# Performance work log

Hardware: AMD Instinct MI355X
Metric: run time of the kernel (lower is better)

Reference implementation:

```python
import jax, jax.numpy as jnp
from jax import lax
import numpy as np

DN = ('NCHW', 'OIHW', 'NCHW')
PAD = [(1, 1), (1, 1)]  # padding=1 each side
STRIDE = (1, 1)


def setup_inputs() -> dict:
    key = jax.random.key(0)
    k0, k1, k2, k3, k4, k5 = jax.random.split(key, 6)
    B, Cin, Cout, H, W, K, FES = 32, 96, 144, 56, 56, 3, 3
    fan_main = Cin * K * K
    fan_extra = FES * K * K
    x = jax.random.normal(k0, (B, Cin, H, W), dtype=jnp.float32)
    extra_inputs = jax.random.normal(k1, (B, Cout * FES), dtype=jnp.float32)
    Wm = jax.random.normal(k2, (Cout, Cin, K, K), dtype=jnp.float32) / np.sqrt(fan_main)
    bm = jax.random.normal(k3, (Cout,), dtype=jnp.float32) * 0.01
    Wx = jax.random.normal(k4, (Cout, FES, K, K), dtype=jnp.float32) / np.sqrt(fan_extra)
    bx = jax.random.normal(k5, (Cout,), dtype=jnp.float32) * 0.01
    return {"x": x, "extra_inputs": extra_inputs, "Wm": Wm, "bm": bm, "Wx": Wx, "bx": bx}


def reference(x, extra_inputs, Wm, bm, Wx, bx):
    # main path: standard conv + bias
    main = lax.conv_general_dilated(x, Wm, STRIDE, PAD, dimension_numbers=DN)
    main = main + bm[None, :, None, None]

    B = x.shape[0]
    Cout, FES, kh, kw = Wx.shape
    H2, W2 = main.shape[2], main.shape[3]

    # Extra path: each extra conv operates on a spatially-constant map, so
    # conv(const_c) = const_c * conv(ones). Compute per-(out,fes)-kernel response
    # to a ones map once (captures zero-padding boundary effects exactly),
    # then combine via a batched einsum — collapsing the per-channel loop.
    ones = jnp.ones((1, 1, x.shape[2], x.shape[3]), dtype=x.dtype)
    M = lax.conv_general_dilated(
        ones, Wx.reshape(Cout * FES, 1, kh, kw), STRIDE, PAD, dimension_numbers=DN
    )  # [1, Cout*FES, H2, W2]
    M = M.reshape(Cout, FES, H2, W2)

    extra = extra_inputs.reshape(B, Cout, FES)
    extra_out = jnp.einsum('bif,ifhw->bihw', extra, M) + bx[None, :, None, None]

    return main + extra_out
```

## Files before the change

kernel.cpp:

```cpp
#include <hip/hip_runtime.h>
#include <hip/hip_bf16.h>

#define B_    32
#define CIN   96
#define COUT  144
#define H_    56
#define W_    56
#define HW    3136
#define NPIX  100352
#define KTOT  864
#define MT    256
#define TAPSZ (COUT*CIN)
#define W2    58
#define PLANE (W2*W2)
#define XTP_SHORTS ((size_t)B_ * PLANE * CIN)

typedef short  short8  __attribute__((ext_vector_type(8)));
typedef float  floatx4 __attribute__((ext_vector_type(4)));

__device__ __forceinline__ unsigned short f2bf(float f) {
    union { float f; unsigned int u; } v; v.f = f;
    unsigned int u = v.u;
    return (unsigned short)((u + 0x7FFFu + ((u >> 16) & 1u)) >> 16);
}

__device__ __forceinline__ void glds16(const void* g, void* l) {
    __builtin_amdgcn_global_load_lds(
        (const __attribute__((address_space(1))) unsigned int*)g,
        (__attribute__((address_space(3))) unsigned int*)l, 16, 0, 0);
}

#define TB 1568
#define WB 486
#define EB 18
#define ZB 342
__global__ __launch_bounds__(256) void prep_all(const float* __restrict__ x,
                                                unsigned short* __restrict__ xTp,
                                                const float* __restrict__ Wm,
                                                unsigned short* __restrict__ Wt,
                                                const float* __restrict__ extra,
                                                const float* __restrict__ Wx,
                                                const float* __restrict__ bm,
                                                const float* __restrict__ bx,
                                                float* __restrict__ E) {
    __shared__ __align__(16) unsigned short tile[64][CIN + 8];
    int blk = blockIdx.x;
    int t = threadIdx.x;
    if (blk < TB) {
        int b   = blk / 49;
        int hw0 = (blk % 49) * 64;
        const float* xb = x + (size_t)b * CIN * HW;
        for (int i = t; i < CIN * 16; i += 256) {
            int ci = i >> 4, seg = i & 15;
            float4 v = *(const float4*)(xb + (size_t)ci * HW + hw0 + seg * 4);
            int hwl = seg * 4;
            tile[hwl + 0][ci] = f2bf(v.x);
            tile[hwl + 1][ci] = f2bf(v.y);
            tile[hwl + 2][ci] = f2bf(v.z);
            tile[hwl + 3][ci] = f2bf(v.w);
        }
        __syncthreads();
        int row = t >> 2, part = t & 3;
        int hw = hw0 + row;
        int h  = hw / W_;
        int w  = hw - h * W_;
        const uint4* s = (const uint4*)&tile[row][part * 24];
        uint4* d = (uint4*)(xTp + ((size_t)((b * W2 + h + 1) * W2 + (w + 1))) * CIN
                                + part * 24);
        d[0] = s[0]; d[1] = s[1]; d[2] = s[2];
    } else if (blk < TB + WB) {
        int i = (blk - TB) * 256 + t;
        int tap = i / 13824;
        int r1  = i - tap * 13824;
        int g   = r1 / 1152;
        int r2  = r1 - g * 1152;
        int co  = r2 >> 3;
        int e   = r2 & 7;
        int ci  = g * 8 + e;
        Wt[i] = f2bf(Wm[((size_t)co * CIN + ci) * 9 + tap]);
    } else if (blk < TB + WB + EB) {
        int i = (blk - TB - WB) * 256 + t;
        int b = i / COUT, co = i - b * COUT;
        float base = bm[co] + bx[co];
        float m[3][3] = {{0,0,0},{0,0,0},{0,0,0}};
        for (int f = 0; f < 3; ++f) {
            float e = extra[(size_t)b * (COUT * 3) + co * 3 + f];
            const float* w = Wx + ((size_t)co * 3 + f) * 9;
            for (int rc = 0; rc < 3; ++rc) {
                int kh0 = (rc == 0) ? 1 : 0;
                int kh1 = (rc == 2) ? 1 : 2;
                for (int cc = 0; cc < 3; ++cc) {
                    int kw0 = (cc == 0) ? 1 : 0;
                    int kw1 = (cc == 2) ? 1 : 2;
                    float s = 0.f;
                    for (int kh = kh0; kh <= kh1; ++kh)
                        for (int kw = kw0; kw <= kw1; ++kw)
                            s += w[kh * 3 + kw];
                    m[rc][cc] += e * s;
                }
            }
        }
        float* dst = E + (size_t)i * 9;
        for (int rc = 0; rc < 3; ++rc)
            for (int cc = 0; cc < 3; ++cc)
                dst[rc * 3 + cc] = base + m[rc][cc];
    } else {
        int i = (blk - TB - WB - EB) * 256 + t;
        int b = i / 2736;
        int r = i - b * 2736;
        size_t base_b = (size_t)b * PLANE * CIN;
        size_t addr;
        if (r < 696) {
            addr = base_b + (size_t)r * 8;
        } else if (r < 1392) {
            addr = base_b + (size_t)57 * W2 * CIN + (size_t)(r - 696) * 8;
        } else if (r < 2064) {
            int r2 = r - 1392;
            int h = 1 + r2 / 12, u = r2 - (r2 / 12) * 12;
            addr = base_b + (size_t)(h * W2) * CIN + (size_t)u * 8;
        } else {
            int r2 = r - 2064;
            int h = 1 + r2 / 12, u = r2 - (r2 / 12) * 12;
            addr = base_b + (size_t)(h * W2 + 57) * CIN + (size_t)u * 8;
        }
        *(short8*)(xTp + addr) = (short8){0, 0, 0, 0, 0, 0, 0, 0};
    }
}

__global__ __launch_bounds__(256, 2) void conv_gemm(const unsigned short* __restrict__ xTp,
                                                    const unsigned short* __restrict__ Wt,
                                                    const float* __restrict__ E,
                                                    float* __restrict__ out) {
    __shared__ __align__(16) unsigned short Bs[2 * TAPSZ];

    int tid = threadIdx.x;
    int wv = tid >> 6, lane = tid & 63;
    int r16 = lane & 15, q = lane >> 4;
    int pixBase = blockIdx.x * MT;

    floatx4 acc[4][9];
    #pragma unroll
    for (int m = 0; m < 4; ++m)
        #pragma unroll
        for (int n = 0; n < 9; ++n)
            acc[m][n] = (floatx4){0.f, 0.f, 0.f, 0.f};

    int aOff[4];
    #pragma unroll
    for (int ms = 0; ms < 4; ++ms) {
        int p = pixBase + wv * 64 + ms * 16 + r16;
        int b = p / HW;
        int hw = p - b * HW;
        int h = hw / W_;
        int w = hw - h * W_;
        aOff[ms] = ((b * W2 + h + 1) * W2 + (w + 1)) * CIN + q * 8;
    }

    const bool bTail = (tid < 192);

    const unsigned short* BpBase = Bs + (q * COUT + r16) * 8;

    short8 a[4][3];

    {
        const unsigned short* wsrc = Wt;
        #pragma unroll
        for (int j = 0; j < 6; ++j)
            glds16(wsrc + tid * 8 + j * 2048, (void*)(Bs + tid * 8 + j * 2048));
        if (bTail)
            glds16(wsrc + tid * 8 + 6 * 2048, (void*)(Bs + tid * 8 + 6 * 2048));
        const unsigned short* bT = xTp + (ptrdiff_t)((-1 * W2 - 1) * CIN);
        #pragma unroll
        for (int ms = 0; ms < 4; ++ms)
            #pragma unroll
            for (int ks = 0; ks < 3; ++ks)
                a[ms][ks] = *(const short8*)(bT + aOff[ms] + ks * 32);
    }
    __syncthreads();

    #pragma unroll 1
    for (int tap = 0; tap < 9; ++tap) {
        const int cur = tap & 1, nxt = cur ^ 1;
        const bool pf = (tap < 8);

        const int tap2 = tap + (pf ? 1 : 0);
        const int r3   = tap2 / 3;
        const int dh2  = r3 - 1, dw2 = tap2 - r3 * 3 - 1;
        const unsigned short* bT = xTp + (ptrdiff_t)((dh2 * W2 + dw2) * CIN);
        if (pf) {
            const unsigned short* wsrc = Wt + tap2 * TAPSZ;
            unsigned short* bd = Bs + nxt * TAPSZ;
            #pragma unroll
            for (int j = 0; j < 6; ++j)
                glds16(wsrc + tid * 8 + j * 2048, (void*)(bd + tid * 8 + j * 2048));
            if (bTail)
                glds16(wsrc + tid * 8 + 6 * 2048, (void*)(bd + tid * 8 + 6 * 2048));
        }

        const unsigned short* Bp = BpBase + cur * TAPSZ;
        #pragma unroll
        for (int ks = 0; ks < 3; ++ks) {
            #pragma unroll
            for (int n3 = 0; n3 < 3; ++n3) {
                short8 b0 = *(const short8*)(Bp + ks * 4608 + (n3 * 3 + 0) * 128);
                short8 b1 = *(const short8*)(Bp + ks * 4608 + (n3 * 3 + 1) * 128);
                short8 b2 = *(const short8*)(Bp + ks * 4608 + (n3 * 3 + 2) * 128);
                #pragma unroll
                for (int ms = 0; ms < 4; ++ms)
                    acc[ms][n3 * 3 + 0] = __builtin_amdgcn_mfma_f32_16x16x32_bf16(
                        a[ms][ks], b0, acc[ms][n3 * 3 + 0], 0, 0, 0);
                #pragma unroll
                for (int ms = 0; ms < 4; ++ms)
                    acc[ms][n3 * 3 + 1] = __builtin_amdgcn_mfma_f32_16x16x32_bf16(
                        a[ms][ks], b1, acc[ms][n3 * 3 + 1], 0, 0, 0);
                #pragma unroll
                for (int ms = 0; ms < 4; ++ms)
                    acc[ms][n3 * 3 + 2] = __builtin_amdgcn_mfma_f32_16x16x32_bf16(
                        a[ms][ks], b2, acc[ms][n3 * 3 + 2], 0, 0, 0);
            }
            #pragma unroll
            for (int ms = 0; ms < 4; ++ms)
                a[ms][ks] = *(const short8*)(bT + aOff[ms] + ks * 32);
        }

        __syncthreads();
    }

    #pragma unroll
    for (int ms = 0; ms < 4; ++ms) {
        int p0 = pixBase + wv * 64 + ms * 16 + q * 4;
        int b  = p0 / HW;
        int hw0 = p0 - b * HW;
        int h = hw0 / W_;
        int w0 = hw0 - h * W_;
        int rc = (h == 0) ? 0 : ((h == H_ - 1) ? 2 : 1);
        int cc0 = (w0 == 0) ? 0 : ((w0 == W_ - 1) ? 2 : 1);
        int cc1 = (w0 + 1 == W_ - 1) ? 2 : 1;
        int cc2 = (w0 + 2 == W_ - 1) ? 2 : 1;
        int cc3 = (w0 + 3 == W_ - 1) ? 2 : 1;
        const float* Ebase = E + (size_t)b * COUT * 9 + rc * 3;
        float* outB = out + (size_t)b * COUT * HW + hw0;
        #pragma unroll
        for (int n = 0; n < 9; ++n) {
            int co = n * 16 + r16;
            const float* Eb = Ebase + co * 9;
            float4 v;
            v.x = acc[ms][n][0] + Eb[cc0];
            v.y = acc[ms][n][1] + Eb[cc1];
            v.z = acc[ms][n][2] + Eb[cc2];
            v.w = acc[ms][n][3] + Eb[cc3];
            *(float4*)(outB + (size_t)co * HW) = v;
        }
    }
}

extern "C" void kernel_launch(void* const* d_in, const int* in_sizes, int n_in,
                              void* d_out, int out_size, void* d_ws, size_t ws_size,
                              hipStream_t stream) {
    const float* x     = (const float*)d_in[0];
    const float* extra = (const float*)d_in[1];
    const float* Wm    = (const float*)d_in[2];
    const float* bm    = (const float*)d_in[3];
    const float* Wx    = (const float*)d_in[4];
    const float* bx    = (const float*)d_in[5];
    float* out = (float*)d_out;

    const size_t XT_BYTES = XTP_SHORTS * 2;
    const size_t WT_BYTES = (size_t)COUT * KTOT * 2;
    const size_t E_BYTES  = (size_t)B_ * COUT * 9 * 4;
    if (ws_size < XT_BYTES + WT_BYTES + E_BYTES) return;

    unsigned short* xTp = (unsigned short*)d_ws;
    unsigned short* Wt  = (unsigned short*)((char*)d_ws + XT_BYTES);
    float*          E   = (float*)((char*)d_ws + XT_BYTES + WT_BYTES);

    prep_all<<<TB + WB + EB + ZB, 256, 0, stream>>>(x, xTp, Wm, Wt, extra, Wx, bm, bx, E);
    conv_gemm<<<NPIX / MT, 256, 0, stream>>>(xTp, Wt, E, out);
}
```

Before: 150.3 us.

## Use 512-thread blocks with smaller per-wave tiles and double-buffered A registers

Doubles the block size to 8 waves, each now computing 32 pixels instead of 64, so each CU holds more waves for latency hiding while the block tile stays the same. The per-tap A fragments are now held in two register sets (aA/aB) that alternate, so the next tap's global loads are issued before the current tap's MFMAs. The tap loop is unrolled in pairs through a macro, and the final tap skips its barrier. In exchange, each wave reads the full B tile from LDS for half as many MFMAs, which doubles LDS read traffic per unit of compute.

Result: no change. 152.7 us (+1.6%).

```diff
diff --git a/kernel.cpp b/kernel.cpp
--- a/kernel.cpp
+++ b/kernel.cpp
@@ -127,7 +127,53 @@
     }
 }
 
-__global__ __launch_bounds__(256, 2) void conv_gemm(const unsigned short* __restrict__ xTp,
+#define TAP_BODY(TAP, CUR, ACUR, ANXT, PF)                                        \
+    do {                                                                          \
+        if (PF) {                                                                 \
+            const int tap2 = (TAP) + 1;                                           \
+            const int r3   = tap2 / 3;                                            \
+            const int dh2  = r3 - 1, dw2 = tap2 - r3 * 3 - 1;                     \
+            const unsigned short* wsrc = Wt + tap2 * TAPSZ;                       \
+            unsigned short* bd = Bs + (1 - (CUR)) * TAPSZ;                        \
+            _Pragma("unroll")                                                     \
+            for (int j = 0; j < 3; ++j)                                           \
+                glds16(wsrc + (tid + j * 512) * 8,                                \
+                       (void*)(bd + (tid + j * 512) * 8));                        \
+            if (bTail)                                                            \
+                glds16(wsrc + (1536 + tid) * 8, (void*)(bd + (1536 + tid) * 8));  \
+            const unsigned short* bT = xTp + (ptrdiff_t)((dh2 * W2 + dw2) * CIN); \
+            _Pragma("unroll")                                                     \
+            for (int ms = 0; ms < 2; ++ms)                                        \
+                _Pragma("unroll")                                                 \
+                for (int ks = 0; ks < 3; ++ks)                                    \
+                    ANXT[ms][ks] = *(const short8*)(bT + aOff[ms] + ks * 32);     \
+        }                                                                         \
+        const unsigned short* Bp = BpBase + (CUR) * TAPSZ;                        \
+        _Pragma("unroll")                                                         \
+        for (int ks = 0; ks < 3; ++ks) {                                          \
+            _Pragma("unroll")                                                     \
+            for (int n3 = 0; n3 < 3; ++n3) {                                      \
+                short8 b0 = *(const short8*)(Bp + ks * 4608 + (n3 * 3 + 0) * 128);\
+                short8 b1 = *(const short8*)(Bp + ks * 4608 + (n3 * 3 + 1) * 128);\
+                short8 b2 = *(const short8*)(Bp + ks * 4608 + (n3 * 3 + 2) * 128);\
+                _Pragma("unroll")                                                 \
+                for (int ms = 0; ms < 2; ++ms)                                    \
+                    acc[ms][n3 * 3 + 0] = __builtin_amdgcn_mfma_f32_16x16x32_bf16(\
+                        ACUR[ms][ks], b0, acc[ms][n3 * 3 + 0], 0, 0, 0);          \
+                _Pragma("unroll")                                                 \
+                for (int ms = 0; ms < 2; ++ms)                                    \
+                    acc[ms][n3 * 3 + 1] = __builtin_amdgcn_mfma_f32_16x16x32_bf16(\
+                        ACUR[ms][ks], b1, acc[ms][n3 * 3 + 1], 0, 0, 0);          \
+                _Pragma("unroll")                                                 \
+                for (int ms = 0; ms < 2; ++ms)                                    \
+                    acc[ms][n3 * 3 + 2] = __builtin_amdgcn_mfma_f32_16x16x32_bf16(\
+                        ACUR[ms][ks], b2, acc[ms][n3 * 3 + 2], 0, 0, 0);          \
+            }                                                                     \
+        }                                                                         \
+        if (PF) __syncthreads();                                                  \
+    } while (0)
+
+__global__ __launch_bounds__(512, 2) void conv_gemm(const unsigned short* __restrict__ xTp,
                                                     const unsigned short* __restrict__ Wt,
                                                     const float* __restrict__ E,
                                                     float* __restrict__ out) {
@@ -138,17 +184,17 @@
     int r16 = lane & 15, q = lane >> 4;
     int pixBase = blockIdx.x * MT;
 
-    floatx4 acc[4][9];
+    floatx4 acc[2][9];
     #pragma unroll
-    for (int m = 0; m < 4; ++m)
+    for (int m = 0; m < 2; ++m)
         #pragma unroll
         for (int n = 0; n < 9; ++n)
             acc[m][n] = (floatx4){0.f, 0.f, 0.f, 0.f};
 
-    int aOff[4];
+    int aOff[2];
     #pragma unroll
-    for (int ms = 0; ms < 4; ++ms) {
-        int p = pixBase + wv * 64 + ms * 16 + r16;
+    for (int ms = 0; ms < 2; ++ms) {
+        int p = pixBase + wv * 32 + ms * 16 + r16;
         int b = p / HW;
         int hw = p - b * HW;
         int h = hw / W_;
@@ -160,75 +206,35 @@
 
     const unsigned short* BpBase = Bs + (q * COUT + r16) * 8;
 
-    short8 a[4][3];
+    short8 aA[2][3], aB[2][3];
 
     {
         const unsigned short* wsrc = Wt;
         #pragma unroll
-        for (int j = 0; j < 6; ++j)
-            glds16(wsrc + tid * 8 + j * 2048, (void*)(Bs + tid * 8 + j * 2048));
+        for (int j = 0; j < 3; ++j)
+            glds16(wsrc + (tid + j * 512) * 8, (void*)(Bs + (tid + j * 512) * 8));
         if (bTail)
-            glds16(wsrc + tid * 8 + 6 * 2048, (void*)(Bs + tid * 8 + 6 * 2048));
+            glds16(wsrc + (1536 + tid) * 8, (void*)(Bs + (1536 + tid) * 8));
         const unsigned short* bT = xTp + (ptrdiff_t)((-1 * W2 - 1) * CIN);
         #pragma unroll
-        for (int ms = 0; ms < 4; ++ms)
+        for (int ms = 0; ms < 2; ++ms)
             #pragma unroll
             for (int ks = 0; ks < 3; ++ks)
-                a[ms][ks] = *(const short8*)(bT + aOff[ms] + ks * 32);
+                aA[ms][ks] = *(const short8*)(bT + aOff[ms] + ks * 32);
     }
     __syncthreads();
 
     #pragma unroll 1
-    for (int tap = 0; tap < 9; ++tap) {
-        const int cur = tap & 1, nxt = cur ^ 1;
-        const bool pf = (tap < 8);
-
-        const int tap2 = tap + (pf ? 1 : 0);
-        const int r3   = tap2 / 3;
-        const int dh2  = r3 - 1, dw2 = tap2 - r3 * 3 - 1;
-        const unsigned short* bT = xTp + (ptrdiff_t)((dh2 * W2 + dw2) * CIN);
-        if (pf) {
-            const unsigned short* wsrc = Wt + tap2 * TAPSZ;
-            unsigned short* bd = Bs + nxt * TAPSZ;
-            #pragma unroll
-            for (int j = 0; j < 6; ++j)
-                glds16(wsrc + tid * 8 + j * 2048, (void*)(bd + tid * 8 + j * 2048));
-            if (bTail)
-                glds16(wsrc + tid * 8 + 6 * 2048, (void*)(bd + tid * 8 + 6 * 2048));
-        }
-
-        const unsigned short* Bp = BpBase + cur * TAPSZ;
-        #pragma unroll
-        for (int ks = 0; ks < 3; ++ks) {
-            #pragma unroll
-            for (int n3 = 0; n3 < 3; ++n3) {
-                short8 b0 = *(const short8*)(Bp + ks * 4608 + (n3 * 3 + 0) * 128);
-                short8 b1 = *(const short8*)(Bp + ks * 4608 + (n3 * 3 + 1) * 128);
-                short8 b2 = *(const short8*)(Bp + ks * 4608 + (n3 * 3 + 2) * 128);
-                #pragma unroll
-                for (int ms = 0; ms < 4; ++ms)
-                    acc[ms][n3 * 3 + 0] = __builtin_amdgcn_mfma_f32_16x16x32_bf16(
-                        a[ms][ks], b0, acc[ms][n3 * 3 + 0], 0, 0, 0);
-                #pragma unroll
-                for (int ms = 0; ms < 4; ++ms)
-                    acc[ms][n3 * 3 + 1] = __builtin_amdgcn_mfma_f32_16x16x32_bf16(
-                        a[ms][ks], b1, acc[ms][n3 * 3 + 1], 0, 0, 0);
-                #pragma unroll
-                for (int ms = 0; ms < 4; ++ms)
-                    acc[ms][n3 * 3 + 2] = __builtin_amdgcn_mfma_f32_16x16x32_bf16(
-                        a[ms][ks], b2, acc[ms][n3 * 3 + 2], 0, 0, 0);
-            }
-            #pragma unroll
-            for (int ms = 0; ms < 4; ++ms)
-                a[ms][ks] = *(const short8*)(bT + aOff[ms] + ks * 32);
-        }
-
-        __syncthreads();
-    }
+    for (int t2 = 0; t2 < 4; ++t2) {
+        const int tapE = 2 * t2;
+        TAP_BODY(tapE,     0, aA, aB, true);
+        TAP_BODY(tapE + 1, 1, aB, aA, true);
+    }
+    TAP_BODY(8, 0, aA, aB, false);
 
     #pragma unroll
-    for (int ms = 0; ms < 4; ++ms) {
-        int p0 = pixBase + wv * 64 + ms * 16 + q * 4;
+    for (int ms = 0; ms < 2; ++ms) {
+        int p0 = pixBase + wv * 32 + ms * 16 + q * 4;
         int b  = p0 / HW;
         int hw0 = p0 - b * HW;
         int h = hw0 / W_;
@@ -275,5 +281,5 @@
     float*          E   = (float*)((char*)d_ws + XT_BYTES + WT_BYTES);
 
     prep_all<<<TB + WB + EB + ZB, 256, 0, stream>>>(x, xTp, Wm, Wt, extra, Wx, bm, bx, E);
-    conv_gemm<<<NPIX / MT, 256, 0, stream>>>(xTp, Wt, E, out);
-}
+    conv_gemm<<<NPIX / MT, 512, 0, stream>>>(xTp, Wt, E, out);
+}
```

## Stage five weight taps in LDS per 512-thread block to cut barriers

Applied to the files above, without the earlier changes.

The block grows to 512 threads and 512 pixels per tile. Instead of double-buffering one weight tap per iteration, the kernel loads weight taps 0-4 into LDS up front, computes them, then reloads the remaining four taps in a single phase. This drops per-tap barriers and async loads from the inner loop. In exchange it uses about 138KB of LDS, which limits occupancy to one block per CU. The grid also shrinks to 196 blocks, and the mid-kernel weight reload is fully exposed with no overlap.

Result: no change. 152.1 us (+1.2%).

```diff
diff --git a/kernel.cpp b/kernel.cpp
--- a/kernel.cpp
+++ b/kernel.cpp
@@ -9,7 +9,7 @@
 #define HW    3136
 #define NPIX  100352
 #define KTOT  864
-#define MT    256
+#define MT    512
 #define TAPSZ (COUT*CIN)
 #define W2    58
 #define PLANE (W2*W2)
@@ -127,11 +127,40 @@
     }
 }
 
-__global__ __launch_bounds__(256, 2) void conv_gemm(const unsigned short* __restrict__ xTp,
+#define MFMA16(A, B, C) __builtin_amdgcn_mfma_f32_16x16x32_bf16(A, B, C, 0, 0, 0)
+
+#define TAP_COMPUTE(BP, BT, PF)                                                   \
+    do {                                                                          \
+        _Pragma("unroll")                                                         \
+        for (int ks = 0; ks < 3; ++ks) {                                          \
+            _Pragma("unroll")                                                     \
+            for (int n3 = 0; n3 < 3; ++n3) {                                      \
+                short8 b0 = *(const short8*)((BP) + ks * 4608 + (n3 * 3 + 0) * 128);\
+                short8 b1 = *(const short8*)((BP) + ks * 4608 + (n3 * 3 + 1) * 128);\
+                short8 b2 = *(const short8*)((BP) + ks * 4608 + (n3 * 3 + 2) * 128);\
+                _Pragma("unroll")                                                 \
+                for (int ms = 0; ms < 4; ++ms)                                    \
+                    acc[ms][n3 * 3 + 0] = MFMA16(a[ms][ks], b0, acc[ms][n3 * 3 + 0]);\
+                _Pragma("unroll")                                                 \
+                for (int ms = 0; ms < 4; ++ms)                                    \
+                    acc[ms][n3 * 3 + 1] = MFMA16(a[ms][ks], b1, acc[ms][n3 * 3 + 1]);\
+                _Pragma("unroll")                                                 \
+                for (int ms = 0; ms < 4; ++ms)                                    \
+                    acc[ms][n3 * 3 + 2] = MFMA16(a[ms][ks], b2, acc[ms][n3 * 3 + 2]);\
+            }                                                                     \
+            if (PF) {                                                             \
+                _Pragma("unroll")                                                 \
+                for (int ms = 0; ms < 4; ++ms)                                    \
+                    a[ms][ks] = *(const short8*)((BT) + aOff[ms] + ks * 32);      \
+            }                                                                     \
+        }                                                                         \
+    } while (0)
+
+__global__ __launch_bounds__(512, 2) void conv_gemm(const unsigned short* __restrict__ xTp,
                                                     const unsigned short* __restrict__ Wt,
                                                     const float* __restrict__ E,
                                                     float* __restrict__ out) {
-    __shared__ __align__(16) unsigned short Bs[2 * TAPSZ];
+    __shared__ __align__(16) unsigned short Bs[5 * TAPSZ];
 
     int tid = threadIdx.x;
     int wv = tid >> 6, lane = tid & 63;
@@ -156,19 +185,16 @@
         aOff[ms] = ((b * W2 + h + 1) * W2 + (w + 1)) * CIN + q * 8;
     }
 
-    const bool bTail = (tid < 192);
-
     const unsigned short* BpBase = Bs + (q * COUT + r16) * 8;
 
     short8 a[4][3];
 
     {
-        const unsigned short* wsrc = Wt;
-        #pragma unroll
-        for (int j = 0; j < 6; ++j)
-            glds16(wsrc + tid * 8 + j * 2048, (void*)(Bs + tid * 8 + j * 2048));
-        if (bTail)
-            glds16(wsrc + tid * 8 + 6 * 2048, (void*)(Bs + tid * 8 + 6 * 2048));
+        #pragma unroll
+        for (int j = 0; j < 16; ++j)
+            glds16(Wt + (tid + j * 512) * 8, (void*)(Bs + (tid + j * 512) * 8));
+        if (tid < 448)
+            glds16(Wt + (tid + 16 * 512) * 8, (void*)(Bs + (tid + 16 * 512) * 8));
         const unsigned short* bT = xTp + (ptrdiff_t)((-1 * W2 - 1) * CIN);
         #pragma unroll
         for (int ms = 0; ms < 4; ++ms)
@@ -179,51 +205,36 @@
     __syncthreads();
 
     #pragma unroll 1
-    for (int tap = 0; tap < 9; ++tap) {
-        const int cur = tap & 1, nxt = cur ^ 1;
-        const bool pf = (tap < 8);
-
-        const int tap2 = tap + (pf ? 1 : 0);
-        const int r3   = tap2 / 3;
-        const int dh2  = r3 - 1, dw2 = tap2 - r3 * 3 - 1;
-        const unsigned short* bT = xTp + (ptrdiff_t)((dh2 * W2 + dw2) * CIN);
-        if (pf) {
-            const unsigned short* wsrc = Wt + tap2 * TAPSZ;
-            unsigned short* bd = Bs + nxt * TAPSZ;
-            #pragma unroll
-            for (int j = 0; j < 6; ++j)
-                glds16(wsrc + tid * 8 + j * 2048, (void*)(bd + tid * 8 + j * 2048));
-            if (bTail)
-                glds16(wsrc + tid * 8 + 6 * 2048, (void*)(bd + tid * 8 + 6 * 2048));
-        }
-
-        const unsigned short* Bp = BpBase + cur * TAPSZ;
-        #pragma unroll
-        for (int ks = 0; ks < 3; ++ks) {
-            #pragma unroll
-            for (int n3 = 0; n3 < 3; ++n3) {
-                short8 b0 = *(const short8*)(Bp + ks * 4608 + (n3 * 3 + 0) * 128);
-                short8 b1 = *(const short8*)(Bp + ks * 4608 + (n3 * 3 + 1) * 128);
-                short8 b2 = *(const short8*)(Bp + ks * 4608 + (n3 * 3 + 2) * 128);
-                #pragma unroll
-                for (int ms = 0; ms < 4; ++ms)
-                    acc[ms][n3 * 3 + 0] = __builtin_amdgcn_mfma_f32_16x16x32_bf16(
-                        a[ms][ks], b0, acc[ms][n3 * 3 + 0], 0, 0, 0);
-                #pragma unroll
-                for (int ms = 0; ms < 4; ++ms)
-                    acc[ms][n3 * 3 + 1] = __builtin_amdgcn_mfma_f32_16x16x32_bf16(
-                        a[ms][ks], b1, acc[ms][n3 * 3 + 1], 0, 0, 0);
-                #pragma unroll
-                for (int ms = 0; ms < 4; ++ms)
-                    acc[ms][n3 * 3 + 2] = __builtin_amdgcn_mfma_f32_16x16x32_bf16(
-                        a[ms][ks], b2, acc[ms][n3 * 3 + 2], 0, 0, 0);
-            }
-            #pragma unroll
-            for (int ms = 0; ms < 4; ++ms)
-                a[ms][ks] = *(const short8*)(bT + aOff[ms] + ks * 32);
-        }
-
-        __syncthreads();
+    for (int tap = 0; tap < 5; ++tap) {
+        int t1 = tap + 1;
+        int r3 = (t1 * 11) >> 5;
+        const unsigned short* bT = xTp + (ptrdiff_t)(((r3 - 1) * W2 + (t1 - r3 * 3 - 1)) * CIN);
+        const unsigned short* Bp = BpBase + tap * TAPSZ;
+        TAP_COMPUTE(Bp, bT, true);
+    }
+
+    __syncthreads();
+    {
+        const unsigned short* wsrc = Wt + 5 * TAPSZ;
+        #pragma unroll
+        for (int j = 0; j < 13; ++j)
+            glds16(wsrc + (tid + j * 512) * 8, (void*)(Bs + (tid + j * 512) * 8));
+        if (tid < 256)
+            glds16(wsrc + (tid + 13 * 512) * 8, (void*)(Bs + (tid + 13 * 512) * 8));
+    }
+    __syncthreads();
+
+    #pragma unroll 1
+    for (int tap = 5; tap < 8; ++tap) {
+        int t1 = tap + 1;
+        int r3 = (t1 * 11) >> 5;
+        const unsigned short* bT = xTp + (ptrdiff_t)(((r3 - 1) * W2 + (t1 - r3 * 3 - 1)) * CIN);
+        const unsigned short* Bp = BpBase + (tap - 5) * TAPSZ;
+        TAP_COMPUTE(Bp, bT, true);
+    }
+    {
+        const unsigned short* Bp = BpBase + 3 * TAPSZ;
+        TAP_COMPUTE(Bp, xTp, false);
     }
 
     #pragma unroll
@@ -275,5 +286,5 @@
     float*          E   = (float*)((char*)d_ws + XT_BYTES + WT_BYTES);
 
     prep_all<<<TB + WB + EB + ZB, 256, 0, stream>>>(x, xTp, Wm, Wt, extra, Wx, bm, bx, E);
-    conv_gemm<<<NPIX / MT, 256, 0, stream>>>(xTp, Wt, E, out);
-}
+    conv_gemm<<<NPIX / MT, 512, 0, stream>>>(xTp, Wt, E, out);
+}
```

## Halve pixel tile and single-buffer weight tile in LDS to raise occupancy

Applied to the files above, without the earlier changes.

Cuts the per-block pixel tile from 256 to 128, halving the accumulator and A-fragment registers per wave. The weight double buffer in LDS becomes a single buffer that is loaded and synchronised at the top of every tap, and the launch bound goes from 2 to 3 blocks per CU. The goal is more resident waves to hide latency, at the cost of losing the overlap between the next tap's weight prefetch and the MFMAs. It also doubles how many times each block reloads the full weight set, relative to the number of pixels processed.

Measured after the change: 150.1 us. No clear change (-0.1%).

```diff
diff --git a/kernel.cpp b/kernel.cpp
--- a/kernel.cpp
+++ b/kernel.cpp
@@ -9,7 +9,7 @@
 #define HW    3136
 #define NPIX  100352
 #define KTOT  864
-#define MT    256
+#define MT    128
 #define TAPSZ (COUT*CIN)
 #define W2    58
 #define PLANE (W2*W2)
@@ -127,28 +127,30 @@
     }
 }
 
-__global__ __launch_bounds__(256, 2) void conv_gemm(const unsigned short* __restrict__ xTp,
+#define MFMA16(A, B, C) __builtin_amdgcn_mfma_f32_16x16x32_bf16(A, B, C, 0, 0, 0)
+
+__global__ __launch_bounds__(256, 3) void conv_gemm(const unsigned short* __restrict__ xTp,
                                                     const unsigned short* __restrict__ Wt,
                                                     const float* __restrict__ E,
                                                     float* __restrict__ out) {
-    __shared__ __align__(16) unsigned short Bs[2 * TAPSZ];
+    __shared__ __align__(16) unsigned short Bs[TAPSZ];
 
     int tid = threadIdx.x;
     int wv = tid >> 6, lane = tid & 63;
     int r16 = lane & 15, q = lane >> 4;
     int pixBase = blockIdx.x * MT;
 
-    floatx4 acc[4][9];
+    floatx4 acc[2][9];
     #pragma unroll
-    for (int m = 0; m < 4; ++m)
+    for (int m = 0; m < 2; ++m)
         #pragma unroll
         for (int n = 0; n < 9; ++n)
             acc[m][n] = (floatx4){0.f, 0.f, 0.f, 0.f};
 
-    int aOff[4];
+    int aOff[2];
     #pragma unroll
-    for (int ms = 0; ms < 4; ++ms) {
-        int p = pixBase + wv * 64 + ms * 16 + r16;
+    for (int ms = 0; ms < 2; ++ms) {
+        int p = pixBase + wv * 32 + ms * 16 + r16;
         int b = p / HW;
         int hw = p - b * HW;
         int h = hw / W_;
@@ -160,66 +162,51 @@
 
     const unsigned short* BpBase = Bs + (q * COUT + r16) * 8;
 
-    short8 a[4][3];
+    short8 a[2][3];
 
     {
-        const unsigned short* wsrc = Wt;
-        #pragma unroll
-        for (int j = 0; j < 6; ++j)
-            glds16(wsrc + tid * 8 + j * 2048, (void*)(Bs + tid * 8 + j * 2048));
-        if (bTail)
-            glds16(wsrc + tid * 8 + 6 * 2048, (void*)(Bs + tid * 8 + 6 * 2048));
-        const unsigned short* bT = xTp + (ptrdiff_t)((-1 * W2 - 1) * CIN);
-        #pragma unroll
-        for (int ms = 0; ms < 4; ++ms)
+        const unsigned short* bT = xTp - (ptrdiff_t)((W2 + 1) * CIN);
+        #pragma unroll
+        for (int ms = 0; ms < 2; ++ms)
             #pragma unroll
             for (int ks = 0; ks < 3; ++ks)
                 a[ms][ks] = *(const short8*)(bT + aOff[ms] + ks * 32);
     }
-    __syncthreads();
 
     #pragma unroll 1
     for (int tap = 0; tap < 9; ++tap) {
-        const int cur = tap & 1, nxt = cur ^ 1;
-        const bool pf = (tap < 8);
-
-        const int tap2 = tap + (pf ? 1 : 0);
-        const int r3   = tap2 / 3;
-        const int dh2  = r3 - 1, dw2 = tap2 - r3 * 3 - 1;
-        const unsigned short* bT = xTp + (ptrdiff_t)((dh2 * W2 + dw2) * CIN);
-        if (pf) {
-            const unsigned short* wsrc = Wt + tap2 * TAPSZ;
-            unsigned short* bd = Bs + nxt * TAPSZ;
-            #pragma unroll
-            for (int j = 0; j < 6; ++j)
-                glds16(wsrc + tid * 8 + j * 2048, (void*)(bd + tid * 8 + j * 2048));
-            if (bTail)
-                glds16(wsrc + tid * 8 + 6 * 2048, (void*)(bd + tid * 8 + 6 * 2048));
-        }
-
-        const unsigned short* Bp = BpBase + cur * TAPSZ;
+        const unsigned short* wsrc = Wt + tap * TAPSZ;
+        #pragma unroll
+        for (int j = 0; j < 6; ++j)
+            glds16(wsrc + (tid + j * 256) * 8, (void*)(Bs + (tid + j * 256) * 8));
+        if (bTail)
+            glds16(wsrc + (1536 + tid) * 8, (void*)(Bs + (1536 + tid) * 8));
+        __syncthreads();
+
+        const int t1 = (tap < 8) ? tap + 1 : 8;
+        const int r3 = (t1 * 11) >> 5;
+        const unsigned short* bT =
+            xTp + (ptrdiff_t)(((r3 - 1) * W2 + (t1 - r3 * 3 - 1)) * CIN);
+
         #pragma unroll
         for (int ks = 0; ks < 3; ++ks) {
             #pragma unroll
             for (int n3 = 0; n3 < 3; ++n3) {
-                short8 b0 = *(const short8*)(Bp + ks * 4608 + (n3 * 3 + 0) * 128);
-                short8 b1 = *(const short8*)(Bp + ks * 4608 + (n3 * 3 + 1) * 128);
-                short8 b2 = *(const short8*)(Bp + ks * 4608 + (n3 * 3 + 2) * 128);
+                short8 b0 = *(const short8*)(BpBase + ks * 4608 + (n3 * 3 + 0) * 128);
+                short8 b1 = *(const short8*)(BpBase + ks * 4608 + (n3 * 3 + 1) * 128);
+                short8 b2 = *(const short8*)(BpBase + ks * 4608 + (n3 * 3 + 2) * 128);
                 #pragma unroll
-                for (int ms = 0; ms < 4; ++ms)
-                    acc[ms][n3 * 3 + 0] = __builtin_amdgcn_mfma_f32_16x16x32_bf16(
-                        a[ms][ks], b0, acc[ms][n3 * 3 + 0], 0, 0, 0);
+                for (int ms = 0; ms < 2; ++ms)
+                    acc[ms][n3 * 3 + 0] = MFMA16(a[ms][ks], b0, acc[ms][n3 * 3 + 0]);
                 #pragma unroll
-                for (int ms = 0; ms < 4; ++ms)
-                    acc[ms][n3 * 3 + 1] = __builtin_amdgcn_mfma_f32_16x16x32_bf16(
-                        a[ms][ks], b1, acc[ms][n3 * 3 + 1], 0, 0, 0);
+                for (int ms = 0; ms < 2; ++ms)
+                    acc[ms][n3 * 3 + 1] = MFMA16(a[ms][ks], b1, acc[ms][n3 * 3 + 1]);
                 #pragma unroll
-                for (int ms = 0; ms < 4; ++ms)
-                    acc[ms][n3 * 3 + 2] = __builtin_amdgcn_mfma_f32_16x16x32_bf16(
-                        a[ms][ks], b2, acc[ms][n3 * 3 + 2], 0, 0, 0);
+                for (int ms = 0; ms < 2; ++ms)
+                    acc[ms][n3 * 3 + 2] = MFMA16(a[ms][ks], b2, acc[ms][n3 * 3 + 2]);
             }
             #pragma unroll
-            for (int ms = 0; ms < 4; ++ms)
+            for (int ms = 0; ms < 2; ++ms)
                 a[ms][ks] = *(const short8*)(bT + aOff[ms] + ks * 32);
         }
 
@@ -227,8 +214,8 @@
     }
 
     #pragma unroll
-    for (int ms = 0; ms < 4; ++ms) {
-        int p0 = pixBase + wv * 64 + ms * 16 + q * 4;
+    for (int ms = 0; ms < 2; ++ms) {
+        int p0 = pixBase + wv * 32 + ms * 16 + q * 4;
         int b  = p0 / HW;
         int hw0 = p0 - b * HW;
         int h = hw0 / W_;
```
